# Kernel tuning notes

Hardware: AMD Instinct MI355X
Metric: run time of the kernel (lower is better)

The kernel has to match this reference:

```python
import jax, jax.numpy as jnp
import numpy as np

B = 8192
IN = 2048
H = 2048


def setup_inputs() -> dict:
    key = jax.random.key(0)
    ks = jax.random.split(key, 16)
    s_in = 1.0 / np.sqrt(IN)
    s_h = 1.0 / np.sqrt(H)
    inp = {
        "x": jax.random.normal(ks[0], (B, IN), jnp.float32),
        "h": jax.random.normal(ks[1], (B, H), jnp.float32),
        "c": jax.random.normal(ks[2], (B, H), jnp.float32),
        # Linear weights stored torch-style as [out, in]
        "w_xf": jax.random.uniform(ks[3], (H, IN), jnp.float32, -s_in, s_in),
        "w_hf": jax.random.uniform(ks[4], (H, H), jnp.float32, -s_h, s_h),
        "b_f": jax.random.normal(ks[5], (H,), jnp.float32),
        "w_xi": jax.random.uniform(ks[6], (H, IN), jnp.float32, -s_in, s_in),
        "w_hi": jax.random.uniform(ks[7], (H, H), jnp.float32, -s_h, s_h),
        "b_i": jax.random.normal(ks[8], (H,), jnp.float32),
        "w_xo": jax.random.uniform(ks[9], (H, IN), jnp.float32, -s_in, s_in),
        "w_ho": jax.random.uniform(ks[10], (H, H), jnp.float32, -s_h, s_h),
        "b_o": jax.random.normal(ks[11], (H,), jnp.float32),
        "w_xc": jax.random.uniform(ks[12], (H, IN), jnp.float32, -s_in, s_in),
        "w_hc": jax.random.uniform(ks[13], (H, H), jnp.float32, -s_h, s_h),
        "b_c": jax.random.normal(ks[14], (H,), jnp.float32),
    }
    return inp


def reference(x, h, c, w_xf, w_hf, b_f, w_xi, w_hi, b_i,
              w_xo, w_ho, b_o, w_xc, w_hc, b_c):
    # Fuse the 8 small GEMMs into 2 batched GEMMs (x-side, h-side).
    Wx = jnp.concatenate([w_xf, w_xi, w_xo, w_xc], axis=0)  # [4H, IN]
    Wh = jnp.concatenate([w_hf, w_hi, w_ho, w_hc], axis=0)  # [4H, H]
    b = jnp.concatenate([b_f, b_i, b_o, b_c], axis=0)       # [4H]
    gates = x @ Wx.T + h @ Wh.T + b                          # [B, 4H]
    hd = h.shape[-1]
    f = jax.nn.sigmoid(gates[:, 0 * hd:1 * hd])
    i = jax.nn.sigmoid(gates[:, 1 * hd:2 * hd])
    o = jax.nn.sigmoid(gates[:, 2 * hd:3 * hd])
    c_tilde = jnp.tanh(gates[:, 3 * hd:4 * hd])
    c_new = f * c + i * c_tilde
    h_new = o * jnp.tanh(c_new)
    return (h_new, c_new)
```

## Files before the change

kernel.cpp:

```cpp
#include <hip/hip_runtime.h>


typedef __attribute__((ext_vector_type(8))) short short8;
typedef __attribute__((ext_vector_type(8))) __bf16 bf16x8;
typedef __attribute__((ext_vector_type(4))) float f32x4;

#define GLDS(gp, lp)                                                        \
  __builtin_amdgcn_global_load_lds(                                         \
      (const __attribute__((address_space(1))) void*)(gp),                  \
      (__attribute__((address_space(3))) void*)(lp), 16, 0, 0)

__device__ __forceinline__ unsigned short f2bf(float f) {
  unsigned u = __builtin_bit_cast(unsigned, f);
  u = (u + 0x7FFFu + ((u >> 16) & 1u)) >> 16;
  return (unsigned short)u;
}

__global__ void pack_x_kernel(const float* __restrict__ x,
                              const float* __restrict__ h,
                              short* __restrict__ X2) {
  long tid = (long)blockIdx.x * blockDim.x + threadIdx.x;
  long flat = tid * 8;
  int row = (int)(flat >> 12);
  int k = (int)(flat & 4095);
  const float* src = (k < 2048) ? (x + (long)row * 2048 + k)
                                : (h + (long)row * 2048 + (k - 2048));
  float4 a = *(const float4*)src;
  float4 b = *(const float4*)(src + 4);
  short8 o;
  o[0] = (short)f2bf(a.x); o[1] = (short)f2bf(a.y);
  o[2] = (short)f2bf(a.z); o[3] = (short)f2bf(a.w);
  o[4] = (short)f2bf(b.x); o[5] = (short)f2bf(b.y);
  o[6] = (short)f2bf(b.z); o[7] = (short)f2bf(b.w);
  *(short8*)(X2 + flat) = o;
}

__global__ void pack_w_kernel(const float* __restrict__ wxf, const float* __restrict__ wxi,
                              const float* __restrict__ wxo, const float* __restrict__ wxc,
                              const float* __restrict__ whf, const float* __restrict__ whi,
                              const float* __restrict__ who, const float* __restrict__ whc,
                              short* __restrict__ W3) {
  long tid = (long)blockIdx.x * blockDim.x + threadIdx.x;
  long flat = tid * 8;
  int j = (int)(flat >> 12);
  int k = (int)(flat & 4095);
  int hc = ((j >> 6) << 4) | (j & 15);
  int g = (j >> 4) & 3;
  const float* base;
  if (k < 2048) {
    const float* wx = (g == 0) ? wxf : (g == 1) ? wxi : (g == 2) ? wxo : wxc;
    base = wx + (long)hc * 2048 + k;
  } else {
    const float* wh = (g == 0) ? whf : (g == 1) ? whi : (g == 2) ? who : whc;
    base = wh + (long)hc * 2048 + (k - 2048);
  }
  float4 a = *(const float4*)base;
  float4 b = *(const float4*)(base + 4);
  short8 o;
  o[0] = (short)f2bf(a.x); o[1] = (short)f2bf(a.y);
  o[2] = (short)f2bf(a.z); o[3] = (short)f2bf(a.w);
  o[4] = (short)f2bf(b.x); o[5] = (short)f2bf(b.y);
  o[6] = (short)f2bf(b.z); o[7] = (short)f2bf(b.w);
  *(short8*)(W3 + flat) = o;
}

__global__ __launch_bounds__(512, 2) void lstm_fused_gemm(
    const short* __restrict__ X2, const short* __restrict__ W3,
    const float* __restrict__ cin,
    const float* __restrict__ bF, const float* __restrict__ bI,
    const float* __restrict__ bO, const float* __restrict__ bC,
    float* __restrict__ hout, float* __restrict__ cout_) {
  __shared__ __align__(16) short lds[65536];

  const int tid = threadIdx.x;
  const int lane = tid & 63;
  const int w = tid >> 6;
  const int wm = w >> 2;
  const int wn = w & 3;

  const int bid = blockIdx.x;
  const int wg = (bid & 7) * 128 + (bid >> 3);
  const int bM = wg >> 5;
  const int bN = wg & 31;

  const int ci = w * 64 + lane;
  const int r0 = ci >> 2;
  const int ss = (ci & 3) ^ ((r0 >> 1) & 3);
  const short* aRow0 = X2 + ((size_t)(bM * 256 + r0)) * 4096 + ss * 8;
  const short* aRow1 = aRow0 + (size_t)128 * 4096;
  const short* bRow0 = W3 + ((size_t)(bN * 256 + r0)) * 4096 + ss * 8;
  const short* bRow1 = bRow0 + (size_t)128 * 4096;
  const int wOff = w * 1024;

#define STAGE2(q, tt, bb) do {                                               \
    const int _kh = (q) >> 1;                                                \
    const short* _g0; const short* _g1;                                      \
    if ((q) == 0 || (q) == 2) {                                              \
      _g0 = aRow0 + (tt) * 64 + _kh * 32;                                    \
      _g1 = aRow1 + (tt) * 64 + _kh * 32;                                    \
    } else {                                                                 \
      _g0 = bRow0 + (tt) * 64 + _kh * 32;                                    \
      _g1 = bRow1 + (tt) * 64 + _kh * 32;                                    \
    }                                                                        \
    char* _l0 = (char*)lds + (bb) * 65536 + (q) * 16384 + wOff;              \
    GLDS(_g0, _l0);                                                          \
    GLDS(_g1, _l0 + 8192);                                                   \
  } while (0)

  const int lr = lane & 15, hi = lane >> 4;
  const int swz = ((hi ^ ((lr >> 1) & 3)) << 4);
  const int aoff = wm * 8192 + lr * 64 + swz;
  const int boff = 16384 + wn * 4096 + lr * 64 + swz;

#define LDSRD(off) (*(const bf16x8*)((const char*)lds + (off)))
#define MFMA_(a, b, c) __builtin_amdgcn_mfma_f32_16x16x32_bf16((a), (b), (c), 0, 0, 0)

  f32x4 acc[8][4] = {};

  STAGE2(0, 0, 0); STAGE2(1, 0, 0); STAGE2(2, 0, 0); STAGE2(3, 0, 0);
  STAGE2(0, 1, 1); STAGE2(1, 1, 1); STAGE2(2, 1, 1);
  asm volatile("s_waitcnt vmcnt(6)" ::: "memory");
  __builtin_amdgcn_s_barrier();

#pragma unroll 2
  for (int t = 0; t < 64; ++t) {
    const int cur = t & 1, nxt = cur ^ 1;
    const int bo = cur << 16;
    const int t1 = (t + 1) & 63;
    const int t2 = (t + 2) & 63;
    bf16x8 a0[8], a1[8];

#pragma unroll
    for (int m = 0; m < 8; ++m) a0[m] = LDSRD(bo + aoff + m * 1024);
    bf16x8 bq0 = LDSRD(bo + boff + 0 * 1024);
    bf16x8 bq1 = LDSRD(bo + boff + 1 * 1024);
    STAGE2(3, t1, nxt);
    __builtin_amdgcn_s_barrier();
    asm volatile("s_waitcnt lgkmcnt(0)" ::: "memory");
    __builtin_amdgcn_sched_barrier(0);
    __builtin_amdgcn_s_setprio(1);
#pragma unroll
    for (int m = 0; m < 8; ++m) acc[m][0] = MFMA_(a0[m], bq0, acc[m][0]);
#pragma unroll
    for (int m = 0; m < 8; ++m) acc[m][1] = MFMA_(a0[m], bq1, acc[m][1]);
    __builtin_amdgcn_s_setprio(0);
    __builtin_amdgcn_s_barrier();

    bf16x8 bq2 = LDSRD(bo + boff + 2 * 1024);
    bf16x8 bq3 = LDSRD(bo + boff + 3 * 1024);
#pragma unroll
    for (int m = 0; m < 8; ++m) a1[m] = LDSRD(bo + aoff + 32768 + m * 1024);
    STAGE2(0, t2, cur);
    __builtin_amdgcn_s_barrier();
    asm volatile("s_waitcnt lgkmcnt(0)" ::: "memory");
    __builtin_amdgcn_sched_barrier(0);
    __builtin_amdgcn_s_setprio(1);
#pragma unroll
    for (int m = 0; m < 8; ++m) acc[m][2] = MFMA_(a0[m], bq2, acc[m][2]);
#pragma unroll
    for (int m = 0; m < 8; ++m) acc[m][3] = MFMA_(a0[m], bq3, acc[m][3]);
    __builtin_amdgcn_s_setprio(0);
    __builtin_amdgcn_s_barrier();

    bf16x8 cq0 = LDSRD(bo + boff + 32768 + 0 * 1024);
    bf16x8 cq1 = LDSRD(bo + boff + 32768 + 1 * 1024);
    STAGE2(1, t2, cur);
    __builtin_amdgcn_s_barrier();
    asm volatile("s_waitcnt lgkmcnt(0)" ::: "memory");
    __builtin_amdgcn_sched_barrier(0);
    __builtin_amdgcn_s_setprio(1);
#pragma unroll
    for (int m = 0; m < 8; ++m) acc[m][0] = MFMA_(a1[m], cq0, acc[m][0]);
#pragma unroll
    for (int m = 0; m < 8; ++m) acc[m][1] = MFMA_(a1[m], cq1, acc[m][1]);
    __builtin_amdgcn_s_setprio(0);
    __builtin_amdgcn_s_barrier();

    bf16x8 cq2 = LDSRD(bo + boff + 32768 + 2 * 1024);
    bf16x8 cq3 = LDSRD(bo + boff + 32768 + 3 * 1024);
    STAGE2(2, t2, cur);
    __builtin_amdgcn_s_barrier();
    asm volatile("s_waitcnt lgkmcnt(0)" ::: "memory");
    __builtin_amdgcn_sched_barrier(0);
    __builtin_amdgcn_s_setprio(1);
#pragma unroll
    for (int m = 0; m < 8; ++m) acc[m][2] = MFMA_(a1[m], cq2, acc[m][2]);
#pragma unroll
    for (int m = 0; m < 8; ++m) acc[m][3] = MFMA_(a1[m], cq3, acc[m][3]);
    __builtin_amdgcn_s_setprio(0);
    asm volatile("s_waitcnt vmcnt(6)" ::: "memory");
    __builtin_amdgcn_s_barrier();
  }

  const int hc = bN * 64 + wn * 16 + lr;
  const float vbf = bF[hc], vbi = bI[hc], vbo = bO[hc], vbc = bC[hc];
#pragma unroll
  for (int m = 0; m < 8; ++m) {
    const int rbase = bM * 256 + wm * 128 + m * 16 + hi * 4;
#pragma unroll
    for (int v = 0; v < 4; ++v) {
      const size_t idx = (size_t)(rbase + v) * 2048 + hc;
      float gf = acc[m][0][v] + vbf;
      float gi = acc[m][1][v] + vbi;
      float go = acc[m][2][v] + vbo;
      float gc = acc[m][3][v] + vbc;
      float fg = 1.f / (1.f + __expf(-gf));
      float ig = 1.f / (1.f + __expf(-gi));
      float og = 1.f / (1.f + __expf(-go));
      float ct = 2.f / (1.f + __expf(-2.f * gc)) - 1.f;
      float cn = fg * cin[idx] + ig * ct;
      float hn = og * (2.f / (1.f + __expf(-2.f * cn)) - 1.f);
      hout[idx] = hn;
      cout_[idx] = cn;
    }
  }
}

extern "C" void kernel_launch(void* const* d_in, const int* in_sizes, int n_in,
                              void* d_out, int out_size, void* d_ws, size_t ws_size,
                              hipStream_t stream) {
  const float* x    = (const float*)d_in[0];
  const float* h    = (const float*)d_in[1];
  const float* c    = (const float*)d_in[2];
  const float* w_xf = (const float*)d_in[3];
  const float* w_hf = (const float*)d_in[4];
  const float* b_f  = (const float*)d_in[5];
  const float* w_xi = (const float*)d_in[6];
  const float* w_hi = (const float*)d_in[7];
  const float* b_i  = (const float*)d_in[8];
  const float* w_xo = (const float*)d_in[9];
  const float* w_ho = (const float*)d_in[10];
  const float* b_o  = (const float*)d_in[11];
  const float* w_xc = (const float*)d_in[12];
  const float* w_hc = (const float*)d_in[13];
  const float* b_c  = (const float*)d_in[14];

  float* hout  = (float*)d_out;
  float* cout_ = hout + (size_t)8192 * 2048;

  short* X2 = (short*)d_ws;
  short* W3 = X2 + (size_t)8192 * 4096;

  const int packBlocks = (int)(((long)8192 * 4096 / 8) / 256);
  pack_x_kernel<<<packBlocks, 256, 0, stream>>>(x, h, X2);
  pack_w_kernel<<<packBlocks, 256, 0, stream>>>(w_xf, w_xi, w_xo, w_xc,
                                                w_hf, w_hi, w_ho, w_hc, W3);

  lstm_fused_gemm<<<1024, 512, 0, stream>>>(X2, W3, c, b_f, b_i, b_o, b_c,
                                            hout, cout_);
}
```

Baseline: 649.3 us.

## Software-pipeline LDS fragment reads one phase ahead of MFMA clusters

Restructures the GEMM main loop so the LDS reads for each MFMA phase are issued one phase earlier. The next tile's A and B fragments are prefetched from the other buffer at the end of the iteration, and partial lgkmcnt waits replace full drains. The goal is to hide LDS read latency behind MFMA work. In exchange it holds more live registers and adds an extra vmcnt wait to make sure the next buffer has landed before it is read.

```diff
diff --git a/kernel.cpp b/kernel.cpp
--- a/kernel.cpp
+++ b/kernel.cpp
@@ -116,77 +116,83 @@
 #define MFMA_(a, b, c) __builtin_amdgcn_mfma_f32_16x16x32_bf16((a), (b), (c), 0, 0, 0)
 
   f32x4 acc[8][4] = {};
+  bf16x8 a0[8], b01[2];
 
   STAGE2(0, 0, 0); STAGE2(1, 0, 0); STAGE2(2, 0, 0); STAGE2(3, 0, 0);
   STAGE2(0, 1, 1); STAGE2(1, 1, 1); STAGE2(2, 1, 1);
   asm volatile("s_waitcnt vmcnt(6)" ::: "memory");
   __builtin_amdgcn_s_barrier();
+#pragma unroll
+  for (int m = 0; m < 8; ++m) a0[m] = LDSRD(aoff + m * 1024);
+  b01[0] = LDSRD(boff + 0 * 1024);
+  b01[1] = LDSRD(boff + 1 * 1024);
 
 #pragma unroll 2
   for (int t = 0; t < 64; ++t) {
     const int cur = t & 1, nxt = cur ^ 1;
-    const int bo = cur << 16;
+    const int bo = cur << 16, bon = nxt << 16;
     const int t1 = (t + 1) & 63;
     const int t2 = (t + 2) & 63;
-    bf16x8 a0[8], a1[8];
-
-#pragma unroll
-    for (int m = 0; m < 8; ++m) a0[m] = LDSRD(bo + aoff + m * 1024);
-    bf16x8 bq0 = LDSRD(bo + boff + 0 * 1024);
-    bf16x8 bq1 = LDSRD(bo + boff + 1 * 1024);
+
+    bf16x8 b23_0 = LDSRD(bo + boff + 2 * 1024);
+    bf16x8 b23_1 = LDSRD(bo + boff + 3 * 1024);
     STAGE2(3, t1, nxt);
     __builtin_amdgcn_s_barrier();
-    asm volatile("s_waitcnt lgkmcnt(0)" ::: "memory");
-    __builtin_amdgcn_sched_barrier(0);
-    __builtin_amdgcn_s_setprio(1);
-#pragma unroll
-    for (int m = 0; m < 8; ++m) acc[m][0] = MFMA_(a0[m], bq0, acc[m][0]);
-#pragma unroll
-    for (int m = 0; m < 8; ++m) acc[m][1] = MFMA_(a0[m], bq1, acc[m][1]);
-    __builtin_amdgcn_s_setprio(0);
-    __builtin_amdgcn_s_barrier();
-
-    bf16x8 bq2 = LDSRD(bo + boff + 2 * 1024);
-    bf16x8 bq3 = LDSRD(bo + boff + 3 * 1024);
+    asm volatile("s_waitcnt lgkmcnt(2)" ::: "memory");
+    __builtin_amdgcn_sched_barrier(0);
+    __builtin_amdgcn_s_setprio(1);
+#pragma unroll
+    for (int m = 0; m < 8; ++m) acc[m][0] = MFMA_(a0[m], b01[0], acc[m][0]);
+#pragma unroll
+    for (int m = 0; m < 8; ++m) acc[m][1] = MFMA_(a0[m], b01[1], acc[m][1]);
+    __builtin_amdgcn_s_setprio(0);
+    __builtin_amdgcn_s_barrier();
+
+    bf16x8 a1[8];
 #pragma unroll
     for (int m = 0; m < 8; ++m) a1[m] = LDSRD(bo + aoff + 32768 + m * 1024);
+    bf16x8 c01_0 = LDSRD(bo + boff + 32768 + 0 * 1024);
+    bf16x8 c01_1 = LDSRD(bo + boff + 32768 + 1 * 1024);
     STAGE2(0, t2, cur);
     __builtin_amdgcn_s_barrier();
-    asm volatile("s_waitcnt lgkmcnt(0)" ::: "memory");
-    __builtin_amdgcn_sched_barrier(0);
-    __builtin_amdgcn_s_setprio(1);
-#pragma unroll
-    for (int m = 0; m < 8; ++m) acc[m][2] = MFMA_(a0[m], bq2, acc[m][2]);
-#pragma unroll
-    for (int m = 0; m < 8; ++m) acc[m][3] = MFMA_(a0[m], bq3, acc[m][3]);
-    __builtin_amdgcn_s_setprio(0);
-    __builtin_amdgcn_s_barrier();
-
-    bf16x8 cq0 = LDSRD(bo + boff + 32768 + 0 * 1024);
-    bf16x8 cq1 = LDSRD(bo + boff + 32768 + 1 * 1024);
+    asm volatile("s_waitcnt lgkmcnt(10)" ::: "memory");
+    __builtin_amdgcn_sched_barrier(0);
+    __builtin_amdgcn_s_setprio(1);
+#pragma unroll
+    for (int m = 0; m < 8; ++m) acc[m][2] = MFMA_(a0[m], b23_0, acc[m][2]);
+#pragma unroll
+    for (int m = 0; m < 8; ++m) acc[m][3] = MFMA_(a0[m], b23_1, acc[m][3]);
+    __builtin_amdgcn_s_setprio(0);
+    __builtin_amdgcn_s_barrier();
+
+    bf16x8 c23_0 = LDSRD(bo + boff + 32768 + 2 * 1024);
+    bf16x8 c23_1 = LDSRD(bo + boff + 32768 + 3 * 1024);
     STAGE2(1, t2, cur);
     __builtin_amdgcn_s_barrier();
-    asm volatile("s_waitcnt lgkmcnt(0)" ::: "memory");
-    __builtin_amdgcn_sched_barrier(0);
-    __builtin_amdgcn_s_setprio(1);
-#pragma unroll
-    for (int m = 0; m < 8; ++m) acc[m][0] = MFMA_(a1[m], cq0, acc[m][0]);
-#pragma unroll
-    for (int m = 0; m < 8; ++m) acc[m][1] = MFMA_(a1[m], cq1, acc[m][1]);
-    __builtin_amdgcn_s_setprio(0);
-    __builtin_amdgcn_s_barrier();
-
-    bf16x8 cq2 = LDSRD(bo + boff + 32768 + 2 * 1024);
-    bf16x8 cq3 = LDSRD(bo + boff + 32768 + 3 * 1024);
+    asm volatile("s_waitcnt lgkmcnt(2)" ::: "memory");
+    __builtin_amdgcn_sched_barrier(0);
+    __builtin_amdgcn_s_setprio(1);
+#pragma unroll
+    for (int m = 0; m < 8; ++m) acc[m][0] = MFMA_(a1[m], c01_0, acc[m][0]);
+#pragma unroll
+    for (int m = 0; m < 8; ++m) acc[m][1] = MFMA_(a1[m], c01_1, acc[m][1]);
+    __builtin_amdgcn_s_setprio(0);
+    asm volatile("s_waitcnt vmcnt(8)" ::: "memory");
+    __builtin_amdgcn_s_barrier();
+
+#pragma unroll
+    for (int m = 0; m < 8; ++m) a0[m] = LDSRD(bon + aoff + m * 1024);
+    b01[0] = LDSRD(bon + boff + 0 * 1024);
+    b01[1] = LDSRD(bon + boff + 1 * 1024);
     STAGE2(2, t2, cur);
     __builtin_amdgcn_s_barrier();
-    asm volatile("s_waitcnt lgkmcnt(0)" ::: "memory");
-    __builtin_amdgcn_sched_barrier(0);
-    __builtin_amdgcn_s_setprio(1);
-#pragma unroll
-    for (int m = 0; m < 8; ++m) acc[m][2] = MFMA_(a1[m], cq2, acc[m][2]);
-#pragma unroll
-    for (int m = 0; m < 8; ++m) acc[m][3] = MFMA_(a1[m], cq3, acc[m][3]);
+    asm volatile("s_waitcnt lgkmcnt(10)" ::: "memory");
+    __builtin_amdgcn_sched_barrier(0);
+    __builtin_amdgcn_s_setprio(1);
+#pragma unroll
+    for (int m = 0; m < 8; ++m) acc[m][2] = MFMA_(a1[m], c23_0, acc[m][2]);
+#pragma unroll
+    for (int m = 0; m < 8; ++m) acc[m][3] = MFMA_(a1[m], c23_1, acc[m][3]);
     __builtin_amdgcn_s_setprio(0);
     asm volatile("s_waitcnt vmcnt(6)" ::: "memory");
     __builtin_amdgcn_s_barrier();
```

Measured after the change: 645.9 us. About the same (-0.5%).

## Restructure GEMM main loop into 4x4 MFMA sub-tiles with reordered prefetch staging

Applied to the files above, without the earlier changes.

The inner loop now loads 4 A fragments and all 4 B fragments per phase and issues 16 MFMAs over a 4x4 sub-tile, instead of 8 A by 2 B fragments. This lowers live fragment registers (8 bf16x8 instead of up to 18) and reuses each B fragment across two phases. The global-to-LDS staging order and vmcnt wait counts are rearranged: quarters 2 and 3 of the next tile are prefetched in the first phase, and the prologue stages one fewer chunk ahead. The sched_barrier calls are removed, so the compiler may interleave LDS reads with MFMAs, at some risk of load stalls or an incorrect wait count.

```diff
diff --git a/kernel.cpp b/kernel.cpp
--- a/kernel.cpp
+++ b/kernel.cpp
@@ -118,8 +118,8 @@
   f32x4 acc[8][4] = {};
 
   STAGE2(0, 0, 0); STAGE2(1, 0, 0); STAGE2(2, 0, 0); STAGE2(3, 0, 0);
-  STAGE2(0, 1, 1); STAGE2(1, 1, 1); STAGE2(2, 1, 1);
-  asm volatile("s_waitcnt vmcnt(6)" ::: "memory");
+  STAGE2(0, 1, 1); STAGE2(1, 1, 1);
+  asm volatile("s_waitcnt vmcnt(8)" ::: "memory");
   __builtin_amdgcn_s_barrier();
 
 #pragma unroll 2
@@ -128,67 +128,64 @@
     const int bo = cur << 16;
     const int t1 = (t + 1) & 63;
     const int t2 = (t + 2) & 63;
-    bf16x8 a0[8], a1[8];
-
-#pragma unroll
-    for (int m = 0; m < 8; ++m) a0[m] = LDSRD(bo + aoff + m * 1024);
-    bf16x8 bq0 = LDSRD(bo + boff + 0 * 1024);
-    bf16x8 bq1 = LDSRD(bo + boff + 1 * 1024);
+    bf16x8 a[4], b[4];
+
+#pragma unroll
+    for (int i = 0; i < 4; ++i) a[i] = LDSRD(bo + aoff + i * 1024);
+#pragma unroll
+    for (int n = 0; n < 4; ++n) b[n] = LDSRD(bo + boff + n * 1024);
+    STAGE2(2, t1, nxt);
     STAGE2(3, t1, nxt);
     __builtin_amdgcn_s_barrier();
     asm volatile("s_waitcnt lgkmcnt(0)" ::: "memory");
-    __builtin_amdgcn_sched_barrier(0);
-    __builtin_amdgcn_s_setprio(1);
-#pragma unroll
-    for (int m = 0; m < 8; ++m) acc[m][0] = MFMA_(a0[m], bq0, acc[m][0]);
-#pragma unroll
-    for (int m = 0; m < 8; ++m) acc[m][1] = MFMA_(a0[m], bq1, acc[m][1]);
-    __builtin_amdgcn_s_setprio(0);
-    __builtin_amdgcn_s_barrier();
-
-    bf16x8 bq2 = LDSRD(bo + boff + 2 * 1024);
-    bf16x8 bq3 = LDSRD(bo + boff + 3 * 1024);
-#pragma unroll
-    for (int m = 0; m < 8; ++m) a1[m] = LDSRD(bo + aoff + 32768 + m * 1024);
+    __builtin_amdgcn_s_setprio(1);
+#pragma unroll
+    for (int n = 0; n < 4; ++n)
+#pragma unroll
+      for (int i = 0; i < 4; ++i) acc[i][n] = MFMA_(a[i], b[n], acc[i][n]);
+    __builtin_amdgcn_s_setprio(0);
+    __builtin_amdgcn_s_barrier();
+
+#pragma unroll
+    for (int i = 0; i < 4; ++i) a[i] = LDSRD(bo + aoff + (4 + i) * 1024);
+    STAGE2(1, t2, cur);
+    __builtin_amdgcn_s_barrier();
+    asm volatile("s_waitcnt lgkmcnt(0)" ::: "memory");
+    __builtin_amdgcn_s_setprio(1);
+#pragma unroll
+    for (int n = 0; n < 4; ++n)
+#pragma unroll
+      for (int i = 0; i < 4; ++i) acc[4 + i][n] = MFMA_(a[i], b[n], acc[4 + i][n]);
+    __builtin_amdgcn_s_setprio(0);
+    asm volatile("s_waitcnt vmcnt(10)" ::: "memory");
+    __builtin_amdgcn_s_barrier();
+
+#pragma unroll
+    for (int i = 0; i < 4; ++i) a[i] = LDSRD(bo + aoff + 32768 + i * 1024);
+#pragma unroll
+    for (int n = 0; n < 4; ++n) b[n] = LDSRD(bo + boff + 32768 + n * 1024);
     STAGE2(0, t2, cur);
     __builtin_amdgcn_s_barrier();
     asm volatile("s_waitcnt lgkmcnt(0)" ::: "memory");
-    __builtin_amdgcn_sched_barrier(0);
-    __builtin_amdgcn_s_setprio(1);
-#pragma unroll
-    for (int m = 0; m < 8; ++m) acc[m][2] = MFMA_(a0[m], bq2, acc[m][2]);
-#pragma unroll
-    for (int m = 0; m < 8; ++m) acc[m][3] = MFMA_(a0[m], bq3, acc[m][3]);
-    __builtin_amdgcn_s_setprio(0);
-    __builtin_amdgcn_s_barrier();
-
-    bf16x8 cq0 = LDSRD(bo + boff + 32768 + 0 * 1024);
-    bf16x8 cq1 = LDSRD(bo + boff + 32768 + 1 * 1024);
-    STAGE2(1, t2, cur);
-    __builtin_amdgcn_s_barrier();
-    asm volatile("s_waitcnt lgkmcnt(0)" ::: "memory");
-    __builtin_amdgcn_sched_barrier(0);
-    __builtin_amdgcn_s_setprio(1);
-#pragma unroll
-    for (int m = 0; m < 8; ++m) acc[m][0] = MFMA_(a1[m], cq0, acc[m][0]);
-#pragma unroll
-    for (int m = 0; m < 8; ++m) acc[m][1] = MFMA_(a1[m], cq1, acc[m][1]);
-    __builtin_amdgcn_s_setprio(0);
-    __builtin_amdgcn_s_barrier();
-
-    bf16x8 cq2 = LDSRD(bo + boff + 32768 + 2 * 1024);
-    bf16x8 cq3 = LDSRD(bo + boff + 32768 + 3 * 1024);
-    STAGE2(2, t2, cur);
-    __builtin_amdgcn_s_barrier();
-    asm volatile("s_waitcnt lgkmcnt(0)" ::: "memory");
-    __builtin_amdgcn_sched_barrier(0);
-    __builtin_amdgcn_s_setprio(1);
-#pragma unroll
-    for (int m = 0; m < 8; ++m) acc[m][2] = MFMA_(a1[m], cq2, acc[m][2]);
-#pragma unroll
-    for (int m = 0; m < 8; ++m) acc[m][3] = MFMA_(a1[m], cq3, acc[m][3]);
-    __builtin_amdgcn_s_setprio(0);
-    asm volatile("s_waitcnt vmcnt(6)" ::: "memory");
+    __builtin_amdgcn_s_setprio(1);
+#pragma unroll
+    for (int n = 0; n < 4; ++n)
+#pragma unroll
+      for (int i = 0; i < 4; ++i) acc[i][n] = MFMA_(a[i], b[n], acc[i][n]);
+    __builtin_amdgcn_s_setprio(0);
+    __builtin_amdgcn_s_barrier();
+
+#pragma unroll
+    for (int i = 0; i < 4; ++i) a[i] = LDSRD(bo + aoff + 32768 + (4 + i) * 1024);
+    __builtin_amdgcn_s_barrier();
+    asm volatile("s_waitcnt lgkmcnt(0)" ::: "memory");
+    __builtin_amdgcn_s_setprio(1);
+#pragma unroll
+    for (int n = 0; n < 4; ++n)
+#pragma unroll
+      for (int i = 0; i < 4; ++i) acc[4 + i][n] = MFMA_(a[i], b[n], acc[4 + i][n]);
+    __builtin_amdgcn_s_setprio(0);
+    asm volatile("s_waitcnt vmcnt(8)" ::: "memory");
     __builtin_amdgcn_s_barrier();
   }
 
```

Result: faster. 619.2 us (-4.6%).
